# Kernel optimization log

Measured on AMD Instinct MI355X. Metric: run time of the kernel, lower is better.

The kernel has to match this reference:

```python
import jax, jax.numpy as jnp
import numpy as np

B, C, H, W = 32, 64, 64, 64
NUM_CODES = 1024
COMMITMENT_COST = 0.25


def setup_inputs() -> dict:
    key = jax.random.key(0)
    k1, k2 = jax.random.split(key)
    z = jax.random.normal(k1, (B, C, H, W), dtype=jnp.float32)
    # matches nn.Embedding init uniform_(-1/num_codes, 1/num_codes)
    codebook = jax.random.uniform(k2, (NUM_CODES, C), dtype=jnp.float32,
                                  minval=-1.0 / NUM_CODES, maxval=1.0 / NUM_CODES)
    return {"z": z, "codebook": codebook}


def reference(z, codebook):
    # b c h w -> b h w c
    zt = jnp.transpose(z, (0, 2, 3, 1))
    b, h, w, c = zt.shape
    z_flat = zt.reshape(-1, c)  # (N, c)

    # squared L2 distances to each code: ||z||^2 + ||e||^2 - 2 z.e
    d = (jnp.sum(z_flat * z_flat, axis=1, keepdims=True)
         + jnp.sum(codebook * codebook, axis=1)[None, :]
         - 2.0 * z_flat @ codebook.T)  # (N, K)
    indices = jnp.argmin(d, axis=1)  # (N,)

    z_q = codebook[indices].reshape(b, h, w, c)

    codebook_loss = jnp.mean((z_q - jax.lax.stop_gradient(zt)) ** 2)
    commitment_loss = jnp.mean((zt - jax.lax.stop_gradient(z_q)) ** 2)
    loss = codebook_loss + COMMITMENT_COST * commitment_loss

    # straight-through estimator
    z_q_st = zt + jax.lax.stop_gradient(z_q - zt)
    z_q_out = jnp.transpose(z_q_st, (0, 3, 1, 2))  # b h w c -> b c h w
    return z_q_out, loss, indices.reshape(b, h, w)
```

## Files before the change

kernel.cpp:

```cpp
#include <hip/hip_runtime.h>

#define CDIM 64
#define KCODES 1024
#define ZQ_ELEMS (32 * 64 * 64 * 64)
#define NROWS 131072
#define FLT_BIG 3.402823466e38f
#define RPB 128
#define NBLK (NROWS / RPB)
#define CSTRIDE 49
#define DELTA 5e-4f

#define WS_BSQ_OFF 16384
#define WS_E1_OFF  32768

typedef __bf16 bf16x8 __attribute__((ext_vector_type(8)));
typedef float  f32x4  __attribute__((ext_vector_type(4)));

__device__ __forceinline__ float pairwise_sq64(const float* v) {
    float r[8];
    #pragma unroll
    for (int j = 0; j < 8; ++j) r[j] = __fmul_rn(v[j], v[j]);
    #pragma unroll
    for (int m = 1; m < 8; ++m) {
        #pragma unroll
        for (int j = 0; j < 8; ++j)
            r[j] = __fadd_rn(r[j], __fmul_rn(v[8 * m + j], v[8 * m + j]));
    }
    return __fadd_rn(__fadd_rn(__fadd_rn(r[0], r[1]), __fadd_rn(r[2], r[3])),
                     __fadd_rn(__fadd_rn(r[4], r[5]), __fadd_rn(r[6], r[7])));
}

__global__ __launch_bounds__(256) void vq_prep(const float* __restrict__ cb,
                                               float* __restrict__ Bsq,
                                               __bf16* __restrict__ e1) {
    const int k = blockIdx.x * 256 + threadIdx.x;
    const float* __restrict__ ck = cb + k * CDIM;
    float v[CDIM];
    #pragma unroll
    for (int q = 0; q < 16; ++q) {
        float4 t = ((const float4*)ck)[q];
        v[4 * q + 0] = t.x; v[4 * q + 1] = t.y; v[4 * q + 2] = t.z; v[4 * q + 3] = t.w;
    }
    Bsq[k] = pairwise_sq64(v);

    const int t = k >> 4, kin = k & 15;
    bf16x8* F1 = (bf16x8*)e1;
    #pragma unroll
    for (int ks = 0; ks < 2; ++ks) {
        #pragma unroll
        for (int g = 0; g < 4; ++g) {
            bf16x8 a;
            #pragma unroll
            for (int i = 0; i < 8; ++i) a[i] = (__bf16)v[ks * 32 + 8 * g + i];
            F1[(t * 2 + ks) * 64 + ((g << 4) | kin)] = a;
        }
    }
}

#define INS(s, j, accv, Bv, code0) \
    { \
        const float vv = __fmaf_rn(-2.f, (accv), (Bv)); \
        const float kk = __int_as_float((__float_as_int(vv) & 0xFFFFFC00) | (code0)); \
        const float o0 = K0[s][j], o1 = K1[s][j], o2 = K2[s][j]; \
        K0[s][j] = fminf(o0, kk); \
        K1[s][j] = __builtin_amdgcn_fmed3f(o0, o1, kk); \
        K2[s][j] = __builtin_amdgcn_fmed3f(o1, o2, kk); \
    }

#define TILE_COMPUTE(Ea, Eb, code0) \
    { \
        const float Bv = sB[code0]; \
        f32x4 a0 = __builtin_amdgcn_mfma_f32_16x16x32_bf16(zh00, Ea, zero, 0, 0, 0); \
        a0       = __builtin_amdgcn_mfma_f32_16x16x32_bf16(zh01, Eb, a0, 0, 0, 0); \
        f32x4 a1 = __builtin_amdgcn_mfma_f32_16x16x32_bf16(zh10, Ea, zero, 0, 0, 0); \
        a1       = __builtin_amdgcn_mfma_f32_16x16x32_bf16(zh11, Eb, a1, 0, 0, 0); \
        INS(0, 0, a0[0], Bv, code0) INS(0, 1, a0[1], Bv, code0) \
        INS(0, 2, a0[2], Bv, code0) INS(0, 3, a0[3], Bv, code0) \
        INS(1, 0, a1[0], Bv, code0) INS(1, 1, a1[1], Bv, code0) \
        INS(1, 2, a1[2], Bv, code0) INS(1, 3, a1[3], Bv, code0) \
    }

__global__ __launch_bounds__(256, 4) void vq_main(const float* __restrict__ z,
                                                  const float* __restrict__ cb,
                                                  const float* __restrict__ Bsq,
                                                  const __bf16* __restrict__ e1,
                                                  float* __restrict__ zq_out,
                                                  float* __restrict__ idx_out,
                                                  double* __restrict__ part) {
    __shared__ __align__(16) unsigned char sU[25152];
    __shared__ float  sB[KCODES];
    __shared__ double sP2[2];

    const int tid = threadIdx.x;
    const int n0 = blockIdx.x * RPB;
    const int b = n0 >> 12;
    const int hw0 = n0 & 4095;
    const float* __restrict__ zb = z + ((size_t)b << 18) + hw0;

    for (int k = tid; k < KCODES; k += 256) sB[k] = Bsq[k];

    {
        bf16x8* __restrict__ zfw = (bf16x8*)sU;
        const int r = tid & 127;
        const int h = tid >> 7;
        const int w = r >> 5, s = (r >> 4) & 1, li = r & 15;
        #pragma unroll
        for (int g = 0; g < 4; ++g) {
            bf16x8 hi;
            #pragma unroll
            for (int i = 0; i < 8; ++i) {
                const float fv = zb[((size_t)(32 * h + 8 * g + i) << 12) + r];
                hi[i] = (__bf16)fv;
            }
            const int slot = (g << 4) | li;
            zfw[(w * 4 + s * 2 + h) * 65 + slot] = hi;
        }
    }
    __syncthreads();

    const int lane = tid & 63, w = tid >> 6;
    const int g = lane >> 4, li = lane & 15;

    const bf16x8* __restrict__ zf = (const bf16x8*)sU;
    const bf16x8 zh00 = zf[(w * 4 + 0) * 65 + lane];
    const bf16x8 zh01 = zf[(w * 4 + 1) * 65 + lane];
    const bf16x8 zh10 = zf[(w * 4 + 2) * 65 + lane];
    const bf16x8 zh11 = zf[(w * 4 + 3) * 65 + lane];

    float K0[2][4], K1[2][4], K2[2][4];
    #pragma unroll
    for (int s = 0; s < 2; ++s)
        #pragma unroll
        for (int j = 0; j < 4; ++j) { K0[s][j] = FLT_BIG; K1[s][j] = FLT_BIG; K2[s][j] = FLT_BIG; }

    const bf16x8* __restrict__ pe1 = (const bf16x8*)e1 + lane;
    const f32x4 zero = {0.f, 0.f, 0.f, 0.f};

    bf16x8 A1a = pe1[0], A1b = pe1[64];
    int tb = li;

    for (int t = 0; t < 64; t += 2) {
        const int o1 = (t + 1) * 128;
        const int o2 = (t + 2) * 128;
        bf16x8 B1a = pe1[o1], B1b = pe1[o1 + 64];
        TILE_COMPUTE(A1a, A1b, tb)
        A1a = pe1[o2]; A1b = pe1[o2 + 64];
        TILE_COMPUTE(B1a, B1b, tb + 16)
        tb += 32;
    }

    __syncthreads();

    float* __restrict__ sKey = (float*)sU;
    #pragma unroll
    for (int s = 0; s < 2; ++s) {
        #pragma unroll
        for (int j = 0; j < 4; ++j) {
            const int row = 32 * w + 16 * s + 4 * g + j;
            const int base = row * CSTRIDE + li * 3;
            sKey[base + 0] = K0[s][j];
            sKey[base + 1] = K1[s][j];
            sKey[base + 2] = K2[s][j];
        }
    }
    __syncthreads();

    if (tid < RPB) {
        const int r = tid;
        const int n = n0 + r;

        float gmin = FLT_BIG;
        #pragma unroll
        for (int s2 = 0; s2 < 48; ++s2) gmin = fminf(gmin, sKey[r * CSTRIDE + s2]);
        const float thr = gmin + DELTA;

        float zrow[CDIM];
        const float* __restrict__ zp = zb + r;
        #pragma unroll
        for (int c = 0; c < CDIM; ++c) zrow[c] = zp[(size_t)c << 12];
        const float A = pairwise_sq64(zrow);

        float bd = FLT_BIG;
        int bk = 1 << 30;
        for (int s2 = 0; s2 < 48; ++s2) {
            const float kv = sKey[r * CSTRIDE + s2];
            if (kv <= thr) {
                const int k = __float_as_int(kv) & 0x3FF;
                const float4* __restrict__ ek = (const float4*)(cb + (size_t)k * CDIM);
                float m = 0.f;
                #pragma unroll
                for (int q = 0; q < 16; ++q) {
                    float4 e = ek[q];
                    m = __fmaf_rn(zrow[4 * q + 0], e.x, m);
                    m = __fmaf_rn(zrow[4 * q + 1], e.y, m);
                    m = __fmaf_rn(zrow[4 * q + 2], e.z, m);
                    m = __fmaf_rn(zrow[4 * q + 3], e.w, m);
                }
                const float d = __fsub_rn(__fadd_rn(A, sB[k]), __fadd_rn(m, m));
                if (d < bd || (d == bd && k < bk)) { bd = d; bk = k; }
            }
        }

        idx_out[n] = (float)bk;

        const float4* __restrict__ cq = (const float4*)(cb + (size_t)bk * CDIM);
        float* __restrict__ zo = zq_out + ((size_t)b << 18) + hw0 + r;
        float lsum = 0.f;
        #pragma unroll
        for (int q = 0; q < 16; ++q) {
            float4 qv = cq[q];
            zo[(size_t)(4 * q + 0) << 12] = qv.x;
            zo[(size_t)(4 * q + 1) << 12] = qv.y;
            zo[(size_t)(4 * q + 2) << 12] = qv.z;
            zo[(size_t)(4 * q + 3) << 12] = qv.w;
            lsum = fmaf(qv.x - zrow[4 * q + 0], qv.x - zrow[4 * q + 0], lsum);
            lsum = fmaf(qv.y - zrow[4 * q + 1], qv.y - zrow[4 * q + 1], lsum);
            lsum = fmaf(qv.z - zrow[4 * q + 2], qv.z - zrow[4 * q + 2], lsum);
            lsum = fmaf(qv.w - zrow[4 * q + 3], qv.w - zrow[4 * q + 3], lsum);
        }

        double ls = (double)lsum;
        for (int off = 32; off > 0; off >>= 1) ls += __shfl_down(ls, off, 64);
        if ((tid & 63) == 0) sP2[tid >> 6] = ls;
    }
    __syncthreads();
    if (tid == 0) part[blockIdx.x] = sP2[0] + sP2[1];
}

__global__ void vq_finalize(const double* __restrict__ part, float* __restrict__ loss_out) {
    __shared__ double s[16];
    const int tid = threadIdx.x;
    double v = part[tid];
    for (int off = 32; off > 0; off >>= 1) v += __shfl_down(v, off, 64);
    if ((tid & 63) == 0) s[tid >> 6] = v;
    __syncthreads();
    if (tid == 0) {
        double t = 0.0;
        #pragma unroll
        for (int i = 0; i < 16; ++i) t += s[i];
        *loss_out = (float)(1.25 * t / (double)ZQ_ELEMS);
    }
}

extern "C" void kernel_launch(void* const* d_in, const int* in_sizes, int n_in,
                              void* d_out, int out_size, void* d_ws, size_t ws_size,
                              hipStream_t stream) {
    const float* z  = (const float*)d_in[0];
    const float* cb = (const float*)d_in[1];
    float* out  = (float*)d_out;
    float* zq   = out;
    float* loss = out + ZQ_ELEMS;
    float* idx  = out + ZQ_ELEMS + 1;
    char* ws = (char*)d_ws;
    double* part = (double*)ws;
    float* Bsq   = (float*)(ws + WS_BSQ_OFF);
    __bf16* e1   = (__bf16*)(ws + WS_E1_OFF);

    vq_prep<<<4, 256, 0, stream>>>(cb, Bsq, e1);
    vq_main<<<NBLK, 256, 0, stream>>>(z, cb, Bsq, e1, zq, idx, part);
    vq_finalize<<<1, 1024, 0, stream>>>(part, loss);
}
```

Before: 78.54 us.

## Halve rows per block and split codebook scan across wave pairs

Each block now handles 64 rows instead of 128. Each pair of waves shares the same row tile and splits the 1024 codes in half, so every wave scans 512 codes and keeps its own top-3 candidates. The key table doubles to 96 entries per row, and finalize sums twice as many partials. This doubles the block count and shortens each wave's serial MFMA loop, at the cost of twice the z loads per block and twice the candidates to scan in the refinement phase, where only 64 threads are active.

```diff
diff --git a/kernel.cpp b/kernel.cpp
--- a/kernel.cpp
+++ b/kernel.cpp
@@ -5,9 +5,9 @@
 #define ZQ_ELEMS (32 * 64 * 64 * 64)
 #define NROWS 131072
 #define FLT_BIG 3.402823466e38f
-#define RPB 128
+#define RPB 64
 #define NBLK (NROWS / RPB)
-#define CSTRIDE 49
+#define CSTRIDE 97
 #define DELTA 5e-4f
 
 #define WS_BSQ_OFF 16384
@@ -87,7 +87,7 @@
                                                   float* __restrict__ zq_out,
                                                   float* __restrict__ idx_out,
                                                   double* __restrict__ part) {
-    __shared__ __align__(16) unsigned char sU[25152];
+    __shared__ __align__(16) unsigned char sU[24832];
     __shared__ float  sB[KCODES];
     __shared__ double sP2[2];
 
@@ -101,31 +101,33 @@
 
     {
         bf16x8* __restrict__ zfw = (bf16x8*)sU;
-        const int r = tid & 127;
-        const int h = tid >> 7;
-        const int w = r >> 5, s = (r >> 4) & 1, li = r & 15;
-        #pragma unroll
-        for (int g = 0; g < 4; ++g) {
+        const int r = tid & 63;
+        const int hh = tid >> 6;
+        const int H = hh >> 1, G = hh & 1;
+        const int wp = r >> 5, s = (r >> 4) & 1, li = r & 15;
+        #pragma unroll
+        for (int gg = 0; gg < 2; ++gg) {
+            const int g = G * 2 + gg;
             bf16x8 hi;
             #pragma unroll
             for (int i = 0; i < 8; ++i) {
-                const float fv = zb[((size_t)(32 * h + 8 * g + i) << 12) + r];
+                const float fv = zb[((size_t)(32 * H + 8 * g + i) << 12) + r];
                 hi[i] = (__bf16)fv;
             }
-            const int slot = (g << 4) | li;
-            zfw[(w * 4 + s * 2 + h) * 65 + slot] = hi;
+            zfw[(wp * 4 + s * 2 + H) * 65 + ((g << 4) | li)] = hi;
         }
     }
     __syncthreads();
 
     const int lane = tid & 63, w = tid >> 6;
+    const int wp = w >> 1, kh = w & 1;
     const int g = lane >> 4, li = lane & 15;
 
     const bf16x8* __restrict__ zf = (const bf16x8*)sU;
-    const bf16x8 zh00 = zf[(w * 4 + 0) * 65 + lane];
-    const bf16x8 zh01 = zf[(w * 4 + 1) * 65 + lane];
-    const bf16x8 zh10 = zf[(w * 4 + 2) * 65 + lane];
-    const bf16x8 zh11 = zf[(w * 4 + 3) * 65 + lane];
+    const bf16x8 zh00 = zf[(wp * 4 + 0) * 65 + lane];
+    const bf16x8 zh01 = zf[(wp * 4 + 1) * 65 + lane];
+    const bf16x8 zh10 = zf[(wp * 4 + 2) * 65 + lane];
+    const bf16x8 zh11 = zf[(wp * 4 + 3) * 65 + lane];
 
     float K0[2][4], K1[2][4], K2[2][4];
     #pragma unroll
@@ -133,13 +135,13 @@
         #pragma unroll
         for (int j = 0; j < 4; ++j) { K0[s][j] = FLT_BIG; K1[s][j] = FLT_BIG; K2[s][j] = FLT_BIG; }
 
-    const bf16x8* __restrict__ pe1 = (const bf16x8*)e1 + lane;
+    const bf16x8* __restrict__ pe1 = (const bf16x8*)e1 + kh * 4096 + lane;
     const f32x4 zero = {0.f, 0.f, 0.f, 0.f};
 
     bf16x8 A1a = pe1[0], A1b = pe1[64];
-    int tb = li;
-
-    for (int t = 0; t < 64; t += 2) {
+    int tb = (kh << 9) | li;
+
+    for (int t = 0; t < 32; t += 2) {
         const int o1 = (t + 1) * 128;
         const int o2 = (t + 2) * 128;
         bf16x8 B1a = pe1[o1], B1b = pe1[o1 + 64];
@@ -156,8 +158,8 @@
     for (int s = 0; s < 2; ++s) {
         #pragma unroll
         for (int j = 0; j < 4; ++j) {
-            const int row = 32 * w + 16 * s + 4 * g + j;
-            const int base = row * CSTRIDE + li * 3;
+            const int row = 32 * wp + 16 * s + 4 * g + j;
+            const int base = row * CSTRIDE + kh * 48 + li * 3;
             sKey[base + 0] = K0[s][j];
             sKey[base + 1] = K1[s][j];
             sKey[base + 2] = K2[s][j];
@@ -171,7 +173,7 @@
 
         float gmin = FLT_BIG;
         #pragma unroll
-        for (int s2 = 0; s2 < 48; ++s2) gmin = fminf(gmin, sKey[r * CSTRIDE + s2]);
+        for (int s2 = 0; s2 < 96; ++s2) gmin = fminf(gmin, sKey[r * CSTRIDE + s2]);
         const float thr = gmin + DELTA;
 
         float zrow[CDIM];
@@ -182,7 +184,7 @@
 
         float bd = FLT_BIG;
         int bk = 1 << 30;
-        for (int s2 = 0; s2 < 48; ++s2) {
+        for (int s2 = 0; s2 < 96; ++s2) {
             const float kv = sKey[r * CSTRIDE + s2];
             if (kv <= thr) {
                 const int k = __float_as_int(kv) & 0x3FF;
@@ -221,16 +223,16 @@
 
         double ls = (double)lsum;
         for (int off = 32; off > 0; off >>= 1) ls += __shfl_down(ls, off, 64);
-        if ((tid & 63) == 0) sP2[tid >> 6] = ls;
-    }
-    __syncthreads();
-    if (tid == 0) part[blockIdx.x] = sP2[0] + sP2[1];
+        if (tid == 0) sP2[0] = ls;
+    }
+    __syncthreads();
+    if (tid == 0) part[blockIdx.x] = sP2[0];
 }
 
 __global__ void vq_finalize(const double* __restrict__ part, float* __restrict__ loss_out) {
     __shared__ double s[16];
     const int tid = threadIdx.x;
-    double v = part[tid];
+    double v = part[tid] + part[tid + 1024];
     for (int off = 32; off > 0; off >>= 1) v += __shfl_down(v, off, 64);
     if ((tid & 63) == 0) s[tid >> 6] = v;
     __syncthreads();
```

New measurement: 101.6 us. +29.4%, slower.

## Stage codebook tiles through double-buffered LDS and split rescoring across all threads

Applied to the files above, without the earlier changes.

The bf16 codebook tiles are now cooperatively loaded into a double-buffered shared-memory region, with the next tile prefetched while the current one feeds MFMA. Previously each wave read codebook fragments directly from global memory. The exact fp32 rescoring of candidate codes is split across both halves of the block, and the two partial results are merged through shared memory, so 256 threads do this work instead of 128. The cost is a __syncthreads per tile iteration and more LDS per block, which could lower occupancy.

```diff
diff --git a/kernel.cpp b/kernel.cpp
--- a/kernel.cpp
+++ b/kernel.cpp
@@ -12,6 +12,12 @@
 
 #define WS_BSQ_OFF 16384
 #define WS_E1_OFF  32768
+
+#define SK_RD_OFF 25088
+#define SK_RK_OFF (25088 + 1024)
+#define E_OFF     27136
+#define B_OFF     (27136 + 8192)
+#define SU_BYTES  (27136 + 8192 + 4096)
 
 typedef __bf16 bf16x8 __attribute__((ext_vector_type(8)));
 typedef float  f32x4  __attribute__((ext_vector_type(4)));
@@ -87,9 +93,9 @@
                                                   float* __restrict__ zq_out,
                                                   float* __restrict__ idx_out,
                                                   double* __restrict__ part) {
-    __shared__ __align__(16) unsigned char sU[25152];
-    __shared__ float  sB[KCODES];
+    __shared__ __align__(16) unsigned char sU[SU_BYTES];
     __shared__ double sP2[2];
+    float* __restrict__ sB = (float*)(sU + B_OFF);
 
     const int tid = threadIdx.x;
     const int n0 = blockIdx.x * RPB;
@@ -112,9 +118,10 @@
                 const float fv = zb[((size_t)(32 * h + 8 * g + i) << 12) + r];
                 hi[i] = (__bf16)fv;
             }
-            const int slot = (g << 4) | li;
-            zfw[(w * 4 + s * 2 + h) * 65 + slot] = hi;
-        }
+            zfw[(w * 4 + s * 2 + h) * 65 + ((g << 4) | li)] = hi;
+        }
+        *(float4*)(sU + E_OFF + tid * 16) =
+            *(const float4*)((const unsigned char*)e1 + tid * 16);
     }
     __syncthreads();
 
@@ -133,25 +140,26 @@
         #pragma unroll
         for (int j = 0; j < 4; ++j) { K0[s][j] = FLT_BIG; K1[s][j] = FLT_BIG; K2[s][j] = FLT_BIG; }
 
-    const bf16x8* __restrict__ pe1 = (const bf16x8*)e1 + lane;
     const f32x4 zero = {0.f, 0.f, 0.f, 0.f};
 
-    bf16x8 A1a = pe1[0], A1b = pe1[64];
-    int tb = li;
-
-    for (int t = 0; t < 64; t += 2) {
-        const int o1 = (t + 1) * 128;
-        const int o2 = (t + 2) * 128;
-        bf16x8 B1a = pe1[o1], B1b = pe1[o1 + 64];
-        TILE_COMPUTE(A1a, A1b, tb)
-        A1a = pe1[o2]; A1b = pe1[o2 + 64];
-        TILE_COMPUTE(B1a, B1b, tb + 16)
-        tb += 32;
-    }
-
-    __syncthreads();
+    for (int c = 0; c < 32; ++c) {
+        float4 vstage;
+        if (c < 31) {
+            vstage = *(const float4*)((const unsigned char*)e1 + (c + 1) * 4096 + tid * 16);
+        }
+        const bf16x8* __restrict__ buf = (const bf16x8*)(sU + E_OFF + (c & 1) * 4096);
+        const int cb0 = c * 32 + li;
+        TILE_COMPUTE(buf[lane],       buf[64 + lane],  cb0)
+        TILE_COMPUTE(buf[128 + lane], buf[192 + lane], cb0 + 16)
+        if (c < 31) {
+            *(float4*)(sU + E_OFF + ((c + 1) & 1) * 4096 + tid * 16) = vstage;
+        }
+        __syncthreads();
+    }
 
     float* __restrict__ sKey = (float*)sU;
+    float* __restrict__ sRd = (float*)(sU + SK_RD_OFF);
+    int*   __restrict__ sRk = (int*)(sU + SK_RK_OFF);
     #pragma unroll
     for (int s = 0; s < 2; ++s) {
         #pragma unroll
@@ -165,8 +173,9 @@
     }
     __syncthreads();
 
-    if (tid < RPB) {
-        const int r = tid;
+    {
+        const int r = tid & 127;
+        const int half = tid >> 7;
         const int n = n0 + r;
 
         float gmin = FLT_BIG;
@@ -182,7 +191,8 @@
 
         float bd = FLT_BIG;
         int bk = 1 << 30;
-        for (int s2 = 0; s2 < 48; ++s2) {
+        const int sbeg = half * 24;
+        for (int s2 = sbeg; s2 < sbeg + 24; ++s2) {
             const float kv = sKey[r * CSTRIDE + s2];
             if (kv <= thr) {
                 const int k = __float_as_int(kv) & 0x3FF;
@@ -201,27 +211,36 @@
             }
         }
 
-        idx_out[n] = (float)bk;
-
-        const float4* __restrict__ cq = (const float4*)(cb + (size_t)bk * CDIM);
-        float* __restrict__ zo = zq_out + ((size_t)b << 18) + hw0 + r;
-        float lsum = 0.f;
-        #pragma unroll
-        for (int q = 0; q < 16; ++q) {
-            float4 qv = cq[q];
-            zo[(size_t)(4 * q + 0) << 12] = qv.x;
-            zo[(size_t)(4 * q + 1) << 12] = qv.y;
-            zo[(size_t)(4 * q + 2) << 12] = qv.z;
-            zo[(size_t)(4 * q + 3) << 12] = qv.w;
-            lsum = fmaf(qv.x - zrow[4 * q + 0], qv.x - zrow[4 * q + 0], lsum);
-            lsum = fmaf(qv.y - zrow[4 * q + 1], qv.y - zrow[4 * q + 1], lsum);
-            lsum = fmaf(qv.z - zrow[4 * q + 2], qv.z - zrow[4 * q + 2], lsum);
-            lsum = fmaf(qv.w - zrow[4 * q + 3], qv.w - zrow[4 * q + 3], lsum);
-        }
-
-        double ls = (double)lsum;
-        for (int off = 32; off > 0; off >>= 1) ls += __shfl_down(ls, off, 64);
-        if ((tid & 63) == 0) sP2[tid >> 6] = ls;
+        if (half == 1) { sRd[r] = bd; sRk[r] = bk; }
+        __syncthreads();
+
+        if (tid < RPB) {
+            const float d1 = sRd[r];
+            const int   k1 = sRk[r];
+            if (d1 < bd || (d1 == bd && k1 < bk)) { bd = d1; bk = k1; }
+
+            idx_out[n] = (float)bk;
+
+            const float4* __restrict__ cq = (const float4*)(cb + (size_t)bk * CDIM);
+            float* __restrict__ zo = zq_out + ((size_t)b << 18) + hw0 + r;
+            float lsum = 0.f;
+            #pragma unroll
+            for (int q = 0; q < 16; ++q) {
+                float4 qv = cq[q];
+                zo[(size_t)(4 * q + 0) << 12] = qv.x;
+                zo[(size_t)(4 * q + 1) << 12] = qv.y;
+                zo[(size_t)(4 * q + 2) << 12] = qv.z;
+                zo[(size_t)(4 * q + 3) << 12] = qv.w;
+                lsum = fmaf(qv.x - zrow[4 * q + 0], qv.x - zrow[4 * q + 0], lsum);
+                lsum = fmaf(qv.y - zrow[4 * q + 1], qv.y - zrow[4 * q + 1], lsum);
+                lsum = fmaf(qv.z - zrow[4 * q + 2], qv.z - zrow[4 * q + 2], lsum);
+                lsum = fmaf(qv.w - zrow[4 * q + 3], qv.w - zrow[4 * q + 3], lsum);
+            }
+
+            double ls = (double)lsum;
+            for (int off = 32; off > 0; off >>= 1) ls += __shfl_down(ls, off, 64);
+            if ((tid & 63) == 0) sP2[tid >> 6] = ls;
+        }
     }
     __syncthreads();
     if (tid == 0) part[blockIdx.x] = sP2[0] + sP2[1];
```

Result: faster. 69.31 us (-11.8%).
